# Performance work log

Measured on AMD Instinct MI355X. Metric: run time of the kernel, lower is better.

The kernel has to match this reference:

```python
import jax, jax.numpy as jnp
import numpy as np
import math

N_FFT = 1024
HOP = 256
N_FRAMES = 16384
SR = 24000
FFT_BIN = N_FFT // 2 + 1
EPS = 1e-11


def hann(n):
    # torch.hann_window default (periodic=True)
    return 0.5 * (1.0 - jnp.cos(2.0 * jnp.pi * jnp.arange(n, dtype=jnp.float32) / n))


def linear_interp(x, scale):
    # x: [B, T] -> [B, T*scale]; matches F.interpolate(mode='linear', align_corners=False)
    T = x.shape[-1]
    pos = (jnp.arange(T * scale, dtype=jnp.float32) + 0.5) / scale - 0.5
    pos = jnp.clip(pos, 0.0, T - 1.0)
    lo = jnp.floor(pos).astype(jnp.int32)
    hi = jnp.minimum(lo + 1, T - 1)
    frac = pos - lo.astype(jnp.float32)
    return x[:, lo] * (1.0 - frac) + x[:, hi] * frac


def impulse_train(f0, hop_length, sample_rate):
    # f0: [B, n_frames] -> impulse train [B, n_frames*hop]
    f0_up = linear_interp(f0, hop_length)
    phase = jnp.cumsum(f0_up, axis=-1) / sample_rate
    saw = jnp.mod(phase, 1.0)
    imp = saw - jnp.roll(saw, -1, axis=-1) + f0_up / sample_rate
    # original runs under torch.no_grad()
    return jax.lax.stop_gradient(imp)


def stft(x, n_fft, hop, window):
    # torch.stft(center=True, pad_mode='reflect', onesided, normalized=False)
    pad = n_fft // 2
    xp = jnp.pad(x, ((0, 0), (pad, pad)), mode="reflect")
    nf = (xp.shape[-1] - n_fft) // hop + 1
    idx = jnp.arange(nf)[:, None] * hop + jnp.arange(n_fft)[None, :]
    frames = xp[:, idx] * window  # [B, nf, n_fft]
    return jnp.fft.rfft(frames, axis=-1).transpose(0, 2, 1)  # [B, bins, nf]


def istft(S, n_fft, hop, window):
    # torch.istft(center=True): windowed overlap-add, divide by sum of squared windows
    B = S.shape[0]
    frames = jnp.fft.irfft(S.transpose(0, 2, 1), n=n_fft, axis=-1) * window  # [B, nf, n_fft]
    nf = frames.shape[1]
    out_len = n_fft + (nf - 1) * hop
    idx = jnp.arange(nf)[:, None] * hop + jnp.arange(n_fft)[None, :]
    sig = jnp.zeros((B, out_len), frames.dtype).at[:, idx].add(frames)
    wsq = jnp.zeros((out_len,), frames.dtype).at[idx].add(
        jnp.broadcast_to(window * window, (nf, n_fft))
    )
    pad = n_fft // 2
    return sig[:, pad:-pad] / jnp.maximum(wsq[pad:-pad], EPS)


def spectral_envelope_filter(signal, envelope, n_fft, hop):
    w = hann(n_fft)
    S = stft(signal, n_fft, hop, w)[:, :, 1:]  # drop first frame -> [B, bins, n_frames]
    return istft(S * envelope, n_fft, hop, w)


def estimate_minimum_phase(amp):
    # amp: [B, bins, T] real positive envelope; cepstral min-phase along dim 1
    n = (amp.shape[1] - 1) * 2
    cep = jnp.fft.irfft(jnp.log(amp), n=n, axis=1)
    fold = jnp.concatenate(
        [jnp.ones((1,), jnp.float32),
         2.0 * jnp.ones((n // 2 - 1,), jnp.float32),
         jnp.ones((1,), jnp.float32),
         jnp.zeros((n // 2 - 1,), jnp.float32)]
    )
    cep = cep * fold[None, :, None]
    return jnp.exp(jnp.fft.rfft(cep, axis=1))  # complex min-phase spectrum [B, bins, T]


def setup_inputs() -> dict:
    key = jax.random.key(0)
    k1, k2, k3 = jax.random.split(key, 3)
    log_f0 = jnp.full((1, N_FRAMES), math.log(100.0), dtype=jnp.float32)
    spec_env_noi = jax.random.normal(k1, (1, FFT_BIN, N_FRAMES), jnp.float32) - 6.0
    spec_env_per = jax.random.normal(k2, (1, FFT_BIN, N_FRAMES), jnp.float32) - 6.0
    noise = jax.random.normal(k3, (1, HOP * N_FRAMES), jnp.float32)
    return {"log_f0": log_f0, "spec_env_noi": spec_env_noi,
            "spec_env_per": spec_env_per, "noise": noise}


def reference(log_f0, spec_env_noi, spec_env_per, noise):
    pulse = impulse_train(jnp.exp(log_f0), HOP, SR)
    noi = spectral_envelope_filter(noise, jnp.exp(spec_env_noi), N_FFT, HOP)
    per = spectral_envelope_filter(
        pulse, estimate_minimum_phase(jnp.exp(spec_env_per)), N_FFT, HOP
    )
    return noi + per  # [1, (N_FRAMES-1)*HOP]
```

## Files before the change

kernel.cpp:

```cpp
#include <hip/hip_runtime.h>
#include <math.h>

#define L_TOT 4194304
#define NFR   16384
#define OUTN  4194048


__device__ __forceinline__ int lvl_off(int a) {
  return L_TOT - (L_TOT >> (a - 1));
}

__device__ __forceinline__ float f0_up_val(const float* f0arr, int j) {
  float pos = __fadd_rn(__fmul_rn(__fadd_rn((float)j, 0.5f), 1.0f / 256.0f), -0.5f);
  pos = fminf(fmaxf(pos, 0.0f), 16383.0f);
  int lo = (int)pos;
  int hi = min(lo + 1, NFR - 1);
  float frac = __fadd_rn(pos, -(float)lo);
  float a = __fmul_rn(f0arr[lo], __fadd_rn(1.0f, -frac));
  float b = __fmul_rn(f0arr[hi], frac);
  return __fadd_rn(a, b);
}

__device__ float prefix_sum(const float* W, const float* f0arr, int m) {
  float acc = 0.0f;
  bool first = true;
  int pos = 0;
  for (int a = 22; a >= 1; --a) {
    if (m & (1 << a)) {
      float node = W[lvl_off(a) + (pos >> a)];
      acc = first ? node : __fadd_rn(acc, node);
      first = false;
      pos += (1 << a);
    }
  }
  if (m & 1) {
    float node = f0_up_val(f0arr, pos);
    acc = first ? node : __fadd_rn(acc, node);
  }
  return acc;
}

__global__ __launch_bounds__(256) void init_tables(const float* __restrict__ logf0,
                                                   float* __restrict__ W) {
  int g = blockIdx.x * 256 + threadIdx.x;
  float* twc = W + 2 * L_TOT;
  float* tws = twc + 512;
  float* wh  = twc + 1024;
  float* f0arr = twc + 2048;
  if (g < 512) {
    double a = (double)g * 3.14159265358979323846 / 512.0;
    twc[g] = (float)cos(a);
    tws[g] = (float)sin(a);
  }
  if (g < 1024) {
    double a = (double)g * 3.14159265358979323846 / 512.0;
    wh[g] = (float)(0.5 - 0.5 * cos(a));
  }
  if (g >= 2048 && g < 2048 + NFR) {
    f0arr[g - 2048] = (float)exp((double)logf0[g - 2048]);
  }
}

__global__ __launch_bounds__(256) void tree_kernel(float* W) {
  const float* f0arr = W + 2 * L_TOT + 2048;
  __shared__ float A[2048];
  __shared__ float B[1024];
  int tid = threadIdx.x;
  int base = blockIdx.x * 2048;
  for (int i = tid; i < 2048; i += 256) A[i] = f0_up_val(f0arr, base + i);
  __syncthreads();
  float* src = A;
  float* dst = B;
  int cnt = 1024;
  for (int a = 1; a <= 11; ++a) {
    int gbase = base >> a;
    for (int i = tid; i < cnt; i += 256) {
      float v = __fadd_rn(src[2 * i], src[2 * i + 1]);
      dst[i] = v;
      if (a >= 10) W[lvl_off(a) + gbase + i] = v;
    }
    __syncthreads();
    float* tmp = src; src = dst; dst = tmp;
    cnt >>= 1;
  }
}

__global__ __launch_bounds__(256) void tree_top_kernel(float* W) {
  __shared__ float A[2048];
  __shared__ float B[1024];
  int tid = threadIdx.x;
  for (int i = tid; i < 2048; i += 256) A[i] = W[lvl_off(11) + i];
  __syncthreads();
  float* src = A;
  float* dst = B;
  int cnt = 1024;
  for (int a = 12; a <= 22; ++a) {
    for (int i = tid; i < cnt; i += 256) {
      float v = __fadd_rn(src[2 * i], src[2 * i + 1]);
      dst[i] = v;
      W[lvl_off(a) + i] = v;
    }
    __syncthreads();
    float* tmp = src; src = dst; dst = tmp;
    cnt >>= 1;
  }
}

__global__ __launch_bounds__(256) void pulse_kernel(float* W) {
  const float* f0arr = W + 2 * L_TOT + 2048;
  __shared__ float f0v[1024];
  __shared__ float Tl[1022];
  __shared__ float P[1026];
  int tid = threadIdx.x;
  int base = blockIdx.x * 1024;

  for (int c = 0; c < 4; ++c)
    f0v[tid + 256 * c] = f0_up_val(f0arr, base + tid + 256 * c);
  __syncthreads();
  Tl[tid]       = __fadd_rn(f0v[2 * tid], f0v[2 * tid + 1]);
  Tl[256 + tid] = __fadd_rn(f0v[512 + 2 * tid], f0v[512 + 2 * tid + 1]);
  __syncthreads();
  Tl[512 + tid] = __fadd_rn(Tl[2 * tid], Tl[2 * tid + 1]);
  __syncthreads();
  if (tid < 128) Tl[768 + tid]  = __fadd_rn(Tl[512 + 2 * tid], Tl[512 + 2 * tid + 1]);
  __syncthreads();
  if (tid < 64)  Tl[896 + tid]  = __fadd_rn(Tl[768 + 2 * tid], Tl[768 + 2 * tid + 1]);
  __syncthreads();
  if (tid < 32)  Tl[960 + tid]  = __fadd_rn(Tl[896 + 2 * tid], Tl[896 + 2 * tid + 1]);
  __syncthreads();
  if (tid < 16)  Tl[992 + tid]  = __fadd_rn(Tl[960 + 2 * tid], Tl[960 + 2 * tid + 1]);
  __syncthreads();
  if (tid < 8)   Tl[1008 + tid] = __fadd_rn(Tl[992 + 2 * tid], Tl[992 + 2 * tid + 1]);
  __syncthreads();
  if (tid < 4)   Tl[1016 + tid] = __fadd_rn(Tl[1008 + 2 * tid], Tl[1008 + 2 * tid + 1]);
  __syncthreads();
  if (tid < 2)   Tl[1020 + tid] = __fadd_rn(Tl[1016 + 2 * tid], Tl[1016 + 2 * tid + 1]);
  __syncthreads();

  float accT = 0.0f;
  bool firstT = true;
  {
    int pos = 0;
    for (int a = 22; a >= 10; --a) {
      if (base & (1 << a)) {
        float node = W[lvl_off(a) + (pos >> a)];
        accT = firstT ? node : __fadd_rn(accT, node);
        firstT = false;
        pos += (1 << a);
      }
    }
  }

  for (int c = 0; c < 4; ++c) {
    int r = 4 * tid + 1 + c;
    if (r <= 1023) {
      float acc = accT;
      bool first = firstT;
      int lpos = 0;
      for (int a = 9; a >= 1; --a) {
        if (r & (1 << a)) {
          float node = Tl[1024 - (1024 >> (a - 1)) + (lpos >> a)];
          acc = first ? node : __fadd_rn(acc, node);
          first = false;
          lpos += (1 << a);
        }
      }
      if (r & 1) {
        float node = f0v[lpos];
        acc = first ? node : __fadd_rn(acc, node);
      }
      P[r] = acc;
    } else {
      P[1024] = prefix_sum(W, f0arr, base + 1024);
    }
  }
  if (tid == 0) {
    int m2 = base + 1025;
    P[1025] = (m2 <= L_TOT) ? prefix_sum(W, f0arr, m2) : 0.0f;
  }
  __syncthreads();

  float o[4];
  for (int c = 0; c < 4; ++c) {
    int i = base + 4 * tid + c;
    float P1 = P[4 * tid + 1 + c];
    float P2 = (i == L_TOT - 1) ? prefix_sum(W, f0arr, 1)
                                : P[4 * tid + 2 + c];
    float t1 = __fdiv_rn(P1, 24000.0f);
    float saw1 = __fadd_rn(t1, -floorf(t1));
    float t2 = __fdiv_rn(P2, 24000.0f);
    float saw2 = __fadd_rn(t2, -floorf(t2));
    float cc = __fdiv_rn(f0v[4 * tid + c], 24000.0f);
    o[c] = __fadd_rn(__fadd_rn(saw1, -saw2), cc);
  }
  *(float4*)&W[L_TOT + base + 4 * tid] = make_float4(o[0], o[1], o[2], o[3]);
}

template <int DIR>
__device__ void fft1024_r4(float2* X, float2* P2buf, const float2* tw) {
  int tid = threadIdx.x;
  float2* S = X;
  float2* D = P2buf;
  __syncthreads();
#pragma unroll
  for (int s = 0; s < 5; ++s) {
    int m = 1 << (2 * s);
    int b = tid;
    int t = b & ~(m - 1);
    float2 twu = tw[t];
    float2 twv = tw[2 * t];
    float ur = twu.x, ui = (DIR > 0) ? twu.y : -twu.y;
    float vr = twv.x, vi = (DIR > 0) ? twv.y : -twv.y;
    float w3r = ur * vr - ui * vi;
    float w3i = ur * vi + ui * vr;
    float2 x0 = S[b], x1 = S[b + 256], x2 = S[b + 512], x3 = S[b + 768];
    float s0r = x0.x + x2.x, s0i = x0.y + x2.y;
    float s1r = x1.x + x3.x, s1i = x1.y + x3.y;
    float d0r = x0.x - x2.x, d0i = x0.y - x2.y;
    float e1r = x1.x - x3.x, e1i = x1.y - x3.y;
    float ser = (DIR > 0) ? -e1i : e1i;
    float sei = (DIR > 0) ? e1r : -e1r;
    int d0 = b + 3 * t;
    D[d0] = make_float2(s0r + s1r, s0i + s1i);
    float t1r = d0r + ser, t1i = d0i + sei;
    D[d0 + m] = make_float2(t1r * ur - t1i * ui, t1r * ui + t1i * ur);
    float t2r = s0r - s1r, t2i = s0i - s1i;
    D[d0 + 2 * m] = make_float2(t2r * vr - t2i * vi, t2r * vi + t2i * vr);
    float t3r = d0r - ser, t3i = d0i - sei;
    D[d0 + 3 * m] = make_float2(t3r * w3r - t3i * w3i, t3r * w3i + t3i * w3r);
    __syncthreads();
    float2* tmp = S; S = D; D = tmp;
  }
}

__device__ __forceinline__ float hann_w(int i, const float2* tw) {
  float c = (i == 512) ? -1.0f : ((i < 512) ? tw[i].x : tw[1024 - i].x);
  return 0.5f - 0.5f * c;
}

__device__ __forceinline__ void combine_one(int k, float An, const float2* Y, float2* H) {
  int k2 = (1024 - k) & 1023;
  float2 z = Y[k], mm = Y[k2];
  float Ar = 0.5f * (z.x + mm.x), Ai = 0.5f * (z.y - mm.y);
  float Br = 0.5f * (z.y + mm.y), Bi = 0.5f * (mm.x - z.x);
  float2 h = H[k];
  H[k] = make_float2(Br * h.x - Bi * h.y + Ar * An,
                     Br * h.y + Bi * h.x + Ai * An);
}

__global__ __launch_bounds__(256) void column_kernel(
    const float* __restrict__ noise,
    const float* __restrict__ envn,
    const float* __restrict__ envp,
    const float* __restrict__ W,
    float* __restrict__ out) {
  __shared__ float2 F[1024], Y[1024];
  __shared__ float2 hA[513], hB[513];
  __shared__ float2 tw[512];
  int tid = threadIdx.x;
  int bid = blockIdx.x;
  int g = (bid & 7) * 1024 + (bid >> 3);
  int fA = 2 * g;
  const float* pulse = W + L_TOT;
  const float* gtab = W + 2 * L_TOT;

  for (int i = tid; i < 512; i += 256) tw[i] = make_float2(gtab[i], gtab[512 + i]);
  for (int k = tid; k < 513; k += 256) {
    float2 e = *(const float2*)&envp[k * NFR + fA];
    hA[k] = e;
  }
  __syncthreads();

  for (int i = tid; i < 1024; i += 256) {
    int k = (i <= 512) ? i : 1024 - i;
    F[i] = hA[k];
  }
  fft1024_r4<+1>(F, Y, tw);
  {
    float2 a0 = Y[tid], a1 = Y[tid + 256], a2 = Y[tid + 512];
    float s0 = (tid == 0) ? (1.0f / 1024.0f) : (2.0f / 1024.0f);
    F[tid] = make_float2(a0.x * s0, a0.y * s0);
    F[tid + 256] = make_float2(a1.x * (2.0f / 1024.0f), a1.y * (2.0f / 1024.0f));
    F[tid + 512] = (tid == 0) ? make_float2(a2.x * (1.0f / 1024.0f),
                                            a2.y * (1.0f / 1024.0f))
                              : make_float2(0.0f, 0.0f);
    F[tid + 768] = make_float2(0.0f, 0.0f);
  }
  fft1024_r4<-1>(F, Y, tw);
  for (int k = tid; k < 513; k += 256) {
    int k2 = (1024 - k) & 1023;
    float2 z = Y[k], mm = Y[k2];
    float GAr = 0.5f * (z.x + mm.x), GAi = 0.5f * (z.y - mm.y);
    float GBr = 0.5f * (z.y + mm.y), GBi = 0.5f * (mm.x - z.x);
    float er = expf(GAr);
    float si, co;
    sincosf(GAi, &si, &co);
    hA[k] = make_float2(er * co, er * si);
    er = expf(GBr);
    sincosf(GBi, &si, &co);
    hB[k] = make_float2(er * co, er * si);
  }

  for (int i = tid; i < 1024; i += 256) {
    int q = 256 * fA - 256 + i;
    if (q < 0) q = -q;
    else if (q >= L_TOT) q = 2 * L_TOT - 2 - q;
    float wv = hann_w(i, tw);
    F[i] = make_float2(noise[q] * wv, pulse[q] * wv);
  }
  fft1024_r4<-1>(F, Y, tw);
  float2 eA0 = *(const float2*)&envn[tid * NFR + fA];
  combine_one(tid, expf(eA0.x), Y, hA);
  float2 eA1 = *(const float2*)&envn[(tid + 256) * NFR + fA];
  combine_one(tid + 256, expf(eA1.x), Y, hA);
  float2 eA2 = make_float2(0.0f, 0.0f);
  if (tid == 0) {
    eA2 = *(const float2*)&envn[512 * NFR + fA];
    combine_one(512, expf(eA2.x), Y, hA);
  }

  for (int i = tid; i < 1024; i += 256) {
    int q = 256 * fA + i;
    if (q >= L_TOT) q = 2 * L_TOT - 2 - q;
    float wv = hann_w(i, tw);
    F[i] = make_float2(noise[q] * wv, pulse[q] * wv);
  }
  fft1024_r4<-1>(F, Y, tw);
  combine_one(tid, expf(eA0.y), Y, hB);
  combine_one(tid + 256, expf(eA1.y), Y, hB);
  if (tid == 0) combine_one(512, expf(eA2.y), Y, hB);
  __syncthreads();

  for (int i = tid; i < 1024; i += 256) {
    if (i <= 512) {
      F[i] = make_float2(hA[i].x - hB[i].y, hA[i].y + hB[i].x);
    } else {
      int j = 1024 - i;
      F[i] = make_float2(hA[j].x + hB[j].y, hB[j].x - hA[j].y);
    }
  }
  fft1024_r4<+1>(F, Y, tw);
  for (int i = tid; i < 1024; i += 256) {
    float wv = hann_w(i, tw) * (1.0f / 1536.0f);
    float ya = Y[i].x * wv;
    float yb = Y[i].y * wv;
    int tA = 256 * fA + i - 512;
    if (tA >= 0 && tA < OUTN) atomicAdd(&out[tA], ya);
    int tB = tA + 256;
    if (tB >= 0 && tB < OUTN) atomicAdd(&out[tB], yb);
  }
}

__global__ __launch_bounds__(256) void finalize_kernel(float* __restrict__ out,
                                                       const float* __restrict__ W) {
  const float* wh = W + 2 * L_TOT + 1024;
  int tid = threadIdx.x;
  int t = (blockIdx.x == 0) ? tid : (OUTN - 256 + tid);
  int p = t + 512;
  int jmin = max(0, (p - 768) >> 8);
  int jmax = min(NFR - 1, p >> 8);
  float wsq = 0.0f;
  for (int j = jmin; j <= jmax; ++j) {
    float w = wh[p - 256 * j];
    wsq += w * w;
  }
  out[t] = out[t] * (1.5f / fmaxf(wsq, 1e-11f));
}

extern "C" void kernel_launch(void* const* d_in, const int* in_sizes, int n_in,
                              void* d_out, int out_size, void* d_ws, size_t ws_size,
                              hipStream_t stream) {
  const float* logf0 = (const float*)d_in[0];
  const float* envn  = (const float*)d_in[1];
  const float* envp  = (const float*)d_in[2];
  const float* noise = (const float*)d_in[3];
  float* out = (float*)d_out;
  float* W = (float*)d_ws;

  init_tables<<<dim3(72), dim3(256), 0, stream>>>(logf0, W);
  tree_kernel<<<dim3(2048), dim3(256), 0, stream>>>(W);
  tree_top_kernel<<<dim3(1), dim3(256), 0, stream>>>(W);
  pulse_kernel<<<dim3(L_TOT / 1024), dim3(256), 0, stream>>>(W);
  hipMemsetAsync(d_out, 0, (size_t)out_size * sizeof(float), stream);
  column_kernel<<<dim3(NFR / 2), dim3(256), 0, stream>>>(noise, envn, envp, W, out);
  finalize_kernel<<<dim3(2), dim3(256), 0, stream>>>(out, W);
}
```

Before: 265.3 us.

## Process 4096 samples per pulse block with register prefix sums and shrink twiddle table

The pulse kernel now handles 4096 samples per block, with 16 samples per thread. The lower levels of the prefix tree are built in registers, which cuts shared-memory passes, barriers and the number of tree levels written to global memory. The FFT computes its second twiddle by squaring the first instead of loading it, and the shared twiddle table is reduced to a quarter period, with the Hann window derived through symmetry. Register pressure rises and there are fewer pulse blocks, and the recomputed twiddles may differ slightly in rounding.

```diff
diff --git a/kernel.cpp b/kernel.cpp
--- a/kernel.cpp
+++ b/kernel.cpp
@@ -77,7 +77,7 @@
     for (int i = tid; i < cnt; i += 256) {
       float v = __fadd_rn(src[2 * i], src[2 * i + 1]);
       dst[i] = v;
-      if (a >= 10) W[lvl_off(a) + gbase + i] = v;
+      if (a == 11) W[lvl_off(11) + gbase + i] = v;
     }
     __syncthreads();
     float* tmp = src; src = dst; dst = tmp;
@@ -108,40 +108,43 @@
 
 __global__ __launch_bounds__(256) void pulse_kernel(float* W) {
   const float* f0arr = W + 2 * L_TOT + 2048;
-  __shared__ float f0v[1024];
-  __shared__ float Tl[1022];
-  __shared__ float P[1026];
-  int tid = threadIdx.x;
-  int base = blockIdx.x * 1024;
-
-  for (int c = 0; c < 4; ++c)
-    f0v[tid + 256 * c] = f0_up_val(f0arr, base + tid + 256 * c);
-  __syncthreads();
-  Tl[tid]       = __fadd_rn(f0v[2 * tid], f0v[2 * tid + 1]);
-  Tl[256 + tid] = __fadd_rn(f0v[512 + 2 * tid], f0v[512 + 2 * tid + 1]);
-  __syncthreads();
-  Tl[512 + tid] = __fadd_rn(Tl[2 * tid], Tl[2 * tid + 1]);
-  __syncthreads();
-  if (tid < 128) Tl[768 + tid]  = __fadd_rn(Tl[512 + 2 * tid], Tl[512 + 2 * tid + 1]);
-  __syncthreads();
-  if (tid < 64)  Tl[896 + tid]  = __fadd_rn(Tl[768 + 2 * tid], Tl[768 + 2 * tid + 1]);
-  __syncthreads();
-  if (tid < 32)  Tl[960 + tid]  = __fadd_rn(Tl[896 + 2 * tid], Tl[896 + 2 * tid + 1]);
-  __syncthreads();
-  if (tid < 16)  Tl[992 + tid]  = __fadd_rn(Tl[960 + 2 * tid], Tl[960 + 2 * tid + 1]);
-  __syncthreads();
-  if (tid < 8)   Tl[1008 + tid] = __fadd_rn(Tl[992 + 2 * tid], Tl[992 + 2 * tid + 1]);
-  __syncthreads();
-  if (tid < 4)   Tl[1016 + tid] = __fadd_rn(Tl[1008 + 2 * tid], Tl[1008 + 2 * tid + 1]);
-  __syncthreads();
-  if (tid < 2)   Tl[1020 + tid] = __fadd_rn(Tl[1016 + 2 * tid], Tl[1016 + 2 * tid + 1]);
+  __shared__ float Tl[510];
+  __shared__ float P[4100];
+  int tid = threadIdx.x;
+  int base = blockIdx.x * 4096;
+
+  float v[16];
+#pragma unroll
+  for (int c = 0; c < 16; ++c) v[c] = f0_up_val(f0arr, base + 16 * tid + c);
+  float s2[8], s4[4], s8[2];
+#pragma unroll
+  for (int j = 0; j < 8; ++j) s2[j] = __fadd_rn(v[2 * j], v[2 * j + 1]);
+#pragma unroll
+  for (int j = 0; j < 4; ++j) s4[j] = __fadd_rn(s2[2 * j], s2[2 * j + 1]);
+  s8[0] = __fadd_rn(s4[0], s4[1]);
+  s8[1] = __fadd_rn(s4[2], s4[3]);
+  Tl[tid] = __fadd_rn(s8[0], s8[1]);
+  __syncthreads();
+  if (tid < 128) Tl[256 + tid] = __fadd_rn(Tl[2 * tid], Tl[2 * tid + 1]);
+  __syncthreads();
+  if (tid < 64)  Tl[384 + tid] = __fadd_rn(Tl[256 + 2 * tid], Tl[256 + 2 * tid + 1]);
+  __syncthreads();
+  if (tid < 32)  Tl[448 + tid] = __fadd_rn(Tl[384 + 2 * tid], Tl[384 + 2 * tid + 1]);
+  __syncthreads();
+  if (tid < 16)  Tl[480 + tid] = __fadd_rn(Tl[448 + 2 * tid], Tl[448 + 2 * tid + 1]);
+  __syncthreads();
+  if (tid < 8)   Tl[496 + tid] = __fadd_rn(Tl[480 + 2 * tid], Tl[480 + 2 * tid + 1]);
+  __syncthreads();
+  if (tid < 4)   Tl[504 + tid] = __fadd_rn(Tl[496 + 2 * tid], Tl[496 + 2 * tid + 1]);
+  __syncthreads();
+  if (tid < 2)   Tl[508 + tid] = __fadd_rn(Tl[504 + 2 * tid], Tl[504 + 2 * tid + 1]);
   __syncthreads();
 
   float accT = 0.0f;
   bool firstT = true;
   {
     int pos = 0;
-    for (int a = 22; a >= 10; --a) {
+    for (int a = 22; a >= 12; --a) {
       if (base & (1 << a)) {
         float node = W[lvl_off(a) + (pos >> a)];
         accT = firstT ? node : __fadd_rn(accT, node);
@@ -150,57 +153,64 @@
       }
     }
   }
-
-  for (int c = 0; c < 4; ++c) {
-    int r = 4 * tid + 1 + c;
-    if (r <= 1023) {
-      float acc = accT;
-      bool first = firstT;
-      int lpos = 0;
-      for (int a = 9; a >= 1; --a) {
-        if (r & (1 << a)) {
-          float node = Tl[1024 - (1024 >> (a - 1)) + (lpos >> a)];
-          acc = first ? node : __fadd_rn(acc, node);
-          first = false;
-          lpos += (1 << a);
-        }
+  float accM = accT;
+  bool firstM = firstT;
+  {
+    int rh = 16 * tid;
+    int lpos = 0;
+    for (int a = 11; a >= 4; --a) {
+      if (rh & (1 << a)) {
+        float node = Tl[512 - (512 >> (a - 4)) + (lpos >> a)];
+        accM = firstM ? node : __fadd_rn(accM, node);
+        firstM = false;
+        lpos += (1 << a);
       }
-      if (r & 1) {
-        float node = f0v[lpos];
-        acc = first ? node : __fadd_rn(acc, node);
-      }
-      P[r] = acc;
-    } else {
-      P[1024] = prefix_sum(W, f0arr, base + 1024);
-    }
-  }
-  if (tid == 0) {
-    int m2 = base + 1025;
-    P[1025] = (m2 <= L_TOT) ? prefix_sum(W, f0arr, m2) : 0.0f;
-  }
-  __syncthreads();
-
-  float o[4];
-  for (int c = 0; c < 4; ++c) {
-    int i = base + 4 * tid + c;
-    float P1 = P[4 * tid + 1 + c];
+    }
+  }
+  if (tid >= 1) P[16 * tid] = accM;
+#pragma unroll
+  for (int c = 1; c <= 15; ++c) {
+    float acc = accM;
+    bool first = firstM;
+    int lp = 0;
+    if (c & 8) { float n = s8[lp >> 3]; acc = first ? n : __fadd_rn(acc, n); first = false; lp += 8; }
+    if (c & 4) { float n = s4[lp >> 2]; acc = first ? n : __fadd_rn(acc, n); first = false; lp += 4; }
+    if (c & 2) { float n = s2[lp >> 1]; acc = first ? n : __fadd_rn(acc, n); first = false; lp += 2; }
+    if (c & 1) { float n = v[lp];       acc = first ? n : __fadd_rn(acc, n); }
+    P[16 * tid + c] = acc;
+  }
+  if (tid == 0) P[4096] = prefix_sum(W, f0arr, base + 4096);
+  if (tid == 1) {
+    int m2 = base + 4097;
+    P[4097] = (m2 <= L_TOT) ? prefix_sum(W, f0arr, m2) : 0.0f;
+  }
+  __syncthreads();
+
+  float o[16];
+#pragma unroll
+  for (int c = 0; c < 16; ++c) {
+    int i = base + 16 * tid + c;
+    float P1 = P[16 * tid + c + 1];
     float P2 = (i == L_TOT - 1) ? prefix_sum(W, f0arr, 1)
-                                : P[4 * tid + 2 + c];
+                                : P[16 * tid + c + 2];
     float t1 = __fdiv_rn(P1, 24000.0f);
     float saw1 = __fadd_rn(t1, -floorf(t1));
     float t2 = __fdiv_rn(P2, 24000.0f);
     float saw2 = __fadd_rn(t2, -floorf(t2));
-    float cc = __fdiv_rn(f0v[4 * tid + c], 24000.0f);
+    float cc = __fdiv_rn(v[c], 24000.0f);
     o[c] = __fadd_rn(__fadd_rn(saw1, -saw2), cc);
   }
-  *(float4*)&W[L_TOT + base + 4 * tid] = make_float4(o[0], o[1], o[2], o[3]);
+#pragma unroll
+  for (int k = 0; k < 4; ++k)
+    *(float4*)&W[L_TOT + base + 16 * tid + 4 * k] =
+        make_float4(o[4 * k], o[4 * k + 1], o[4 * k + 2], o[4 * k + 3]);
 }
 
 template <int DIR>
-__device__ void fft1024_r4(float2* X, float2* P2buf, const float2* tw) {
+__device__ void fft1024_r4(float2* X, float2* Pb, const float2* tw) {
   int tid = threadIdx.x;
   float2* S = X;
-  float2* D = P2buf;
+  float2* D = Pb;
   __syncthreads();
 #pragma unroll
   for (int s = 0; s < 5; ++s) {
@@ -208,9 +218,9 @@
     int b = tid;
     int t = b & ~(m - 1);
     float2 twu = tw[t];
-    float2 twv = tw[2 * t];
     float ur = twu.x, ui = (DIR > 0) ? twu.y : -twu.y;
-    float vr = twv.x, vi = (DIR > 0) ? twv.y : -twv.y;
+    float vr = ur * ur - ui * ui;
+    float vi = 2.0f * ur * ui;
     float w3r = ur * vr - ui * vi;
     float w3i = ur * vi + ui * vr;
     float2 x0 = S[b], x1 = S[b + 256], x2 = S[b + 512], x3 = S[b + 768];
@@ -234,7 +244,8 @@
 }
 
 __device__ __forceinline__ float hann_w(int i, const float2* tw) {
-  float c = (i == 512) ? -1.0f : ((i < 512) ? tw[i].x : tw[1024 - i].x);
+  int j = (i > 512) ? (1024 - i) : i;
+  float c = (j <= 256) ? tw[j].x : -tw[512 - j].x;
   return 0.5f - 0.5f * c;
 }
 
@@ -256,7 +267,7 @@
     float* __restrict__ out) {
   __shared__ float2 F[1024], Y[1024];
   __shared__ float2 hA[513], hB[513];
-  __shared__ float2 tw[512];
+  __shared__ float2 tw[257];
   int tid = threadIdx.x;
   int bid = blockIdx.x;
   int g = (bid & 7) * 1024 + (bid >> 3);
@@ -264,7 +275,7 @@
   const float* pulse = W + L_TOT;
   const float* gtab = W + 2 * L_TOT;
 
-  for (int i = tid; i < 512; i += 256) tw[i] = make_float2(gtab[i], gtab[512 + i]);
+  for (int i = tid; i < 257; i += 256) tw[i] = make_float2(gtab[i], gtab[512 + i]);
   for (int k = tid; k < 513; k += 256) {
     float2 e = *(const float2*)&envp[k * NFR + fA];
     hA[k] = e;
@@ -380,7 +391,7 @@
   init_tables<<<dim3(72), dim3(256), 0, stream>>>(logf0, W);
   tree_kernel<<<dim3(2048), dim3(256), 0, stream>>>(W);
   tree_top_kernel<<<dim3(1), dim3(256), 0, stream>>>(W);
-  pulse_kernel<<<dim3(L_TOT / 1024), dim3(256), 0, stream>>>(W);
+  pulse_kernel<<<dim3(L_TOT / 4096), dim3(256), 0, stream>>>(W);
   hipMemsetAsync(d_out, 0, (size_t)out_size * sizeof(float), stream);
   column_kernel<<<dim3(NFR / 2), dim3(256), 0, stream>>>(noise, envn, envp, W, out);
   finalize_kernel<<<dim3(2), dim3(256), 0, stream>>>(out, W);
```

After: 256.0 us. 1.04x faster.
